# Performance work log

Measured on AMD Instinct MI355X. Metric: run time of the kernel, lower is better.

## Reference

```python
import jax, jax.numpy as jnp
import numpy as np

N_NODES = 100000
N_EDGES = 1600000
IN_DIM = 128
HID = 128


def sage_conv(x, src, dst, W_l, W_r, b, num_nodes):
    # PyG SAGEConv (mean aggregation): out = lin_l(mean_{j in N(i)} x_j) + lin_r(x_i)
    msgs = x[src]                                            # [E, F] gather
    agg = jax.ops.segment_sum(msgs, dst, num_segments=num_nodes)  # [N, F]
    cnt = jax.ops.segment_sum(jnp.ones((src.shape[0],), x.dtype), dst,
                              num_segments=num_nodes)        # [N]
    agg = agg / jnp.maximum(cnt, 1.0)[:, None]               # mean; 0 for isolated nodes
    return agg @ W_l + b + x @ W_r


def setup_inputs() -> dict:
    key = jax.random.key(0)
    ks = jax.random.split(key, 12)
    s_in = 1.0 / np.sqrt(IN_DIM)
    s_h = 1.0 / np.sqrt(HID)
    return {
        "x": jax.random.normal(ks[0], (N_NODES, IN_DIM), jnp.float32),
        "edge_index": jax.random.randint(ks[1], (2, N_EDGES), 0, N_NODES, jnp.int64),
        "Wl1": jax.random.normal(ks[2], (IN_DIM, HID), jnp.float32) * s_in,
        "Wr1": jax.random.normal(ks[3], (IN_DIM, HID), jnp.float32) * s_in,
        "b1": jnp.zeros((HID,), jnp.float32),
        "Wl2": jax.random.normal(ks[4], (HID, HID), jnp.float32) * s_h,
        "Wr2": jax.random.normal(ks[5], (HID, HID), jnp.float32) * s_h,
        "b2": jnp.zeros((HID,), jnp.float32),
        "Wp": jax.random.normal(ks[6], (HID, 1), jnp.float32) * s_h,
        "bp": jnp.zeros((1,), jnp.float32),
        "Wd": jax.random.normal(ks[7], (HID, 1), jnp.float32) * s_h,
        "bd": jnp.zeros((1,), jnp.float32),
    }


def reference(x, edge_index, Wl1, Wr1, b1, Wl2, Wr2, b2, Wp, bp, Wd, bd):
    src, dst = edge_index[0], edge_index[1]
    h = jax.nn.relu(sage_conv(x, src, dst, Wl1, Wr1, b1, N_NODES))
    h = jax.nn.relu(sage_conv(h, src, dst, Wl2, Wr2, b2, N_NODES))
    preds = h @ Wp + bp                      # [N, 1]
    diffs = jax.nn.sigmoid(h @ Wd + bd)      # [N, 1]
    return (preds - diffs, preds + diffs)
```

## Files before the change

kernel.cpp:

```cpp
#include <hip/hip_runtime.h>
#include <hip/hip_bf16.h>

#define N_NODES 100000
#define N_EDGES 1600000
#define NBUCK 391
#define BCAP 5120
#define ACHUNK 4096

typedef __bf16 bf16x8 __attribute__((ext_vector_type(8)));
typedef __bf16 bf16x4 __attribute__((ext_vector_type(4)));
typedef float  f32x4  __attribute__((ext_vector_type(4)));
typedef float  f32x2  __attribute__((ext_vector_type(2)));



__global__ __launch_bounds__(512) void zerob_kernel(int* __restrict__ bcnt,
                                                    int* __restrict__ Psent) {
  int t = threadIdx.x;
  if (t < NBUCK) bcnt[t] = 0;
  if (t >= 480) Psent[t - 480] = 0;
}

__global__ __launch_bounds__(256) void partA_kernel(const int* __restrict__ src,
                                                    const int* __restrict__ dst,
                                                    int* __restrict__ bcnt,
                                                    unsigned* __restrict__ packed, int E) {
  __shared__ int hist[NBUCK];
  __shared__ int curs[NBUCK];
  const int t = threadIdx.x;
  for (int i = t; i < NBUCK; i += 256) hist[i] = 0;
  __syncthreads();

  const int base = blockIdx.x * ACHUNK;
  const int lim = min(base + ACHUNK, E);

  int dloc[16], sloc[16];
  int myn = 0;
  for (int i = base + t; i < lim; i += 256) {
    dloc[myn] = dst[i];
    sloc[myn] = src[i];
    ++myn;
  }
  for (int k = 0; k < myn; ++k) atomicAdd(&hist[dloc[k] >> 8], 1);
  __syncthreads();

  for (int i = t; i < NBUCK; i += 256) {
    int h = hist[i];
    curs[i] = (h > 0) ? atomicAdd(&bcnt[i], h) : 0;
  }
  __syncthreads();

  for (int k = 0; k < myn; ++k) {
    int d = dloc[k];
    int b = d >> 8;
    int pos = atomicAdd(&curs[b], 1);
    if (pos < BCAP)
      packed[(size_t)b * BCAP + pos] = ((unsigned)sloc[k] << 8) | (unsigned)(d & 255);
  }
}

__global__ __launch_bounds__(256) void partBh_kernel(const unsigned* __restrict__ packed,
                                                     const int* __restrict__ bcnt,
                                                     int* __restrict__ pcnt,
                                                     int* __restrict__ deg,
                                                     int* __restrict__ pbt, int N) {
  __shared__ int hist[256];
  __shared__ int red[256];
  const int b = blockIdx.x, t = threadIdx.x;
  hist[t] = 0;
  __syncthreads();
  const int ecnt = min(bcnt[b], BCAP);
  const unsigned* pk = packed + (size_t)b * BCAP;
  for (int i = t; i < ecnt; i += 256) atomicAdd(&hist[pk[i] & 255u], 1);
  __syncthreads();
  int c = hist[t];
  int node = b * 256 + t;
  int pc = (node < N) ? ((c + 3) & ~3) : 0;
  if (node < N) { deg[node] = c; pcnt[node] = pc; }
  red[t] = pc;
  __syncthreads();
  for (int d = 128; d > 0; d >>= 1) {
    if (t < d) red[t] += red[t + d];
    __syncthreads();
  }
  if (t == 0) pbt[b] = red[0];
}

__global__ __launch_bounds__(512) void bscan_kernel(const int* __restrict__ pbt,
                                                    int* __restrict__ bbase,
                                                    int* __restrict__ offs, int N) {
  __shared__ int tmp[512];
  int t = threadIdx.x;
  int v = (t < NBUCK) ? pbt[t] : 0;
  int x = v;
  tmp[t] = x;
  __syncthreads();
  for (int d = 1; d < 512; d <<= 1) {
    int y = (t >= d) ? tmp[t - d] : 0;
    __syncthreads();
    x += y;
    tmp[t] = x;
    __syncthreads();
  }
  if (t < NBUCK) bbase[t] = x - v;
  if (t == NBUCK - 1) offs[N] = x;
}

__global__ __launch_bounds__(256) void partBs_kernel(const unsigned* __restrict__ packed,
                                                     const int* __restrict__ bcnt,
                                                     const int* __restrict__ bbase,
                                                     const int* __restrict__ pcnt,
                                                     const int* __restrict__ deg,
                                                     int* __restrict__ offs,
                                                     int* __restrict__ ssrc, int N) {
  __shared__ int scanbuf[256];
  __shared__ int curs[256];
  const int b = blockIdx.x, t = threadIdx.x;
  const int node = b * 256 + t;
  int pc = (node < N) ? pcnt[node] : 0;
  int c  = (node < N) ? deg[node] : 0;
  int x = pc;
  scanbuf[t] = x;
  __syncthreads();
  for (int d = 1; d < 256; d <<= 1) {
    int y = (t >= d) ? scanbuf[t - d] : 0;
    __syncthreads();
    x += y;
    scanbuf[t] = x;
    __syncthreads();
  }
  int excl = x - pc;
  const int obase = bbase[b];
  if (node < N) offs[node] = obase + excl;
  curs[t] = excl;
  __syncthreads();

  const int ecnt = min(bcnt[b], BCAP);
  const unsigned* pk = packed + (size_t)b * BCAP;
  for (int i = t; i < ecnt; i += 256) {
    unsigned p = pk[i];
    int r = atomicAdd(&curs[p & 255u], 1);
    ssrc[obase + r] = (int)(p >> 8);
  }
  for (int j = c; j < pc; ++j) ssrc[obase + excl + j] = N;
}


__global__ __launch_bounds__(256) void wswz_kernel(const float* __restrict__ Wl1,
                                                   const float* __restrict__ Wr1,
                                                   const float* __restrict__ Wl2,
                                                   const float* __restrict__ Wr2,
                                                   __bf16* __restrict__ W1out,
                                                   __bf16* __restrict__ W2out) {
  int gi = blockIdx.x * blockDim.x + threadIdx.x;
  bool L2 = gi >= 32768;
  int i = gi & 32767;
  int j = i & 7;
  int lane = (i >> 3) & 63;
  int c = (i >> 9) & 3;
  int tile = i >> 11;
  int k = c * 32 + ((lane >> 4) * 8) + j;
  int krow = L2 ? (((k & 7) << 4) | (k >> 3)) : k;
  int col = tile * 16 + (lane & 15);
  const float* Wl = L2 ? Wl2 : Wl1;
  const float* Wr = L2 ? Wr2 : Wr1;
  float v = (col < 128) ? Wl[krow * 128 + col] : Wr[krow * 128 + (col - 128)];
  (L2 ? W2out : W1out)[i] = (__bf16)v;
}


template <bool A_IS_F32>
__global__ __launch_bounds__(256) void gemm_kernel(const void* __restrict__ Aptr,
                                                   const __bf16* __restrict__ Wswz,
                                                   const float* __restrict__ bias,
                                                   unsigned char* __restrict__ P,
                                                   __bf16* __restrict__ R, int M) {
  __shared__ __bf16 ldsA[64][136];
  const int t = threadIdx.x;
  const int m0 = blockIdx.x * 64;

  if (A_IS_F32) {
    const float* A = (const float*)Aptr;
#pragma unroll
    for (int it = 0; it < 8; ++it) {
      int row = it * 8 + (t >> 5);
      int col = (t & 31) * 4;
      float4 v = make_float4(0.f, 0.f, 0.f, 0.f);
      if (m0 + row < M) v = *(const float4*)&A[(size_t)(m0 + row) * 128 + col];
      bf16x4 bv;
      bv.x = (__bf16)v.x; bv.y = (__bf16)v.y; bv.z = (__bf16)v.z; bv.w = (__bf16)v.w;
      *(bf16x4*)&ldsA[row][col] = bv;
    }
  } else {
    const __bf16* A = (const __bf16*)Aptr;
#pragma unroll
    for (int it = 0; it < 4; ++it) {
      int row = it * 16 + (t >> 4);
      int col = (t & 15) * 8;
      uint4 v = make_uint4(0u, 0u, 0u, 0u);
      if (m0 + row < M) v = *(const uint4*)&A[(size_t)(m0 + row) * 128 + col];
      *(uint4*)&ldsA[row][col] = v;
    }
  }

  const int lane = t & 63;
  const int w = t >> 6;
  const int q = lane >> 4;
  const int s = lane & 15;

  float breg[8];
#pragma unroll
  for (int j = 0; j < 8; ++j) breg[j] = bias[j * 16 + s];

  __syncthreads();

  f32x4 acc[16];
  f32x4 zero = {0.f, 0.f, 0.f, 0.f};
#pragma unroll
  for (int i = 0; i < 16; ++i) acc[i] = zero;

  const __bf16* arow = &ldsA[w * 16 + s][0];
#pragma unroll
  for (int c = 0; c < 4; ++c) {
    bf16x8 a = *(const bf16x8*)&arow[c * 32 + q * 8];
#pragma unroll
    for (int nt = 0; nt < 16; ++nt) {
      bf16x8 b = *(const bf16x8*)&Wswz[(size_t)(((nt * 4 + c) * 64) + lane) * 8];
      acc[nt] = __builtin_amdgcn_mfma_f32_16x16x32_bf16(a, b, acc[nt], 0, 0, 0);
    }
  }

  const int rbase = m0 + w * 16 + q * 4;
#pragma unroll
  for (int r = 0; r < 4; ++r) {
    int row = rbase + r;
    if (row < M) {
      unsigned lo = 0, hi = 0;
      lo = __builtin_amdgcn_cvt_pk_fp8_f32(acc[0][r], acc[1][r], lo, false);
      lo = __builtin_amdgcn_cvt_pk_fp8_f32(acc[2][r], acc[3][r], lo, true);
      hi = __builtin_amdgcn_cvt_pk_fp8_f32(acc[4][r], acc[5][r], hi, false);
      hi = __builtin_amdgcn_cvt_pk_fp8_f32(acc[6][r], acc[7][r], hi, true);
      uint2 pv; pv.x = lo; pv.y = hi;
      *(uint2*)&P[(size_t)row * 128 + s * 8] = pv;

      bf16x8 o;
#pragma unroll
      for (int j = 0; j < 8; ++j) o[j] = (__bf16)(acc[8 + j][r] + breg[j]);
      *(bf16x8*)&R[(size_t)row * 128 + s * 8] = o;
    }
  }
}


template <bool FINAL>
__global__ __launch_bounds__(256) void agg_kernel(
    const unsigned char* __restrict__ P, const __bf16* R,
    const int* __restrict__ offs, const int* __restrict__ deg,
    const int* __restrict__ ssrc,
    __bf16* H, float* __restrict__ out,
    const float* __restrict__ Wp, const float* __restrict__ Wd,
    const float* __restrict__ bp, const float* __restrict__ bd, int n) {
  int w4 = (int)((blockIdx.x * blockDim.x + threadIdx.x) >> 6);
  int lane = threadIdx.x & 63;
  int g = lane >> 4;
  int s = lane & 15;
  int node = w4 * 4 + g;
  int nc = min(node, n - 1);
  int start = offs[nc];
  int pend = offs[nc + 1];

  f32x2 a01 = {0.f, 0.f}, a23 = {0.f, 0.f}, a45 = {0.f, 0.f}, a67 = {0.f, 0.f};

  const unsigned char* Pb = P + (size_t)s * 8;
  for (int cur = start; cur < pend; cur += 4) {
    uint4 sv = *(const uint4*)&ssrc[cur];
    uint2 v0 = *(const uint2*)(Pb + (size_t)sv.x * 128);
    uint2 v1 = *(const uint2*)(Pb + (size_t)sv.y * 128);
    uint2 v2 = *(const uint2*)(Pb + (size_t)sv.z * 128);
    uint2 v3 = *(const uint2*)(Pb + (size_t)sv.w * 128);
    a01 += __builtin_amdgcn_cvt_pk_f32_fp8(v0.x, false);
    a23 += __builtin_amdgcn_cvt_pk_f32_fp8(v0.x, true);
    a45 += __builtin_amdgcn_cvt_pk_f32_fp8(v0.y, false);
    a67 += __builtin_amdgcn_cvt_pk_f32_fp8(v0.y, true);
    a01 += __builtin_amdgcn_cvt_pk_f32_fp8(v1.x, false);
    a23 += __builtin_amdgcn_cvt_pk_f32_fp8(v1.x, true);
    a45 += __builtin_amdgcn_cvt_pk_f32_fp8(v1.y, false);
    a67 += __builtin_amdgcn_cvt_pk_f32_fp8(v1.y, true);
    a01 += __builtin_amdgcn_cvt_pk_f32_fp8(v2.x, false);
    a23 += __builtin_amdgcn_cvt_pk_f32_fp8(v2.x, true);
    a45 += __builtin_amdgcn_cvt_pk_f32_fp8(v2.y, false);
    a67 += __builtin_amdgcn_cvt_pk_f32_fp8(v2.y, true);
    a01 += __builtin_amdgcn_cvt_pk_f32_fp8(v3.x, false);
    a23 += __builtin_amdgcn_cvt_pk_f32_fp8(v3.x, true);
    a45 += __builtin_amdgcn_cvt_pk_f32_fp8(v3.y, false);
    a67 += __builtin_amdgcn_cvt_pk_f32_fp8(v3.y, true);
  }

  int dg = deg[nc];
  float inv = 1.0f / (float)(dg > 0 ? dg : 1);

  bf16x8 rv = *(const bf16x8*)&R[(size_t)nc * 128 + s * 8];
  float acc[8] = {a01[0], a01[1], a23[0], a23[1], a45[0], a45[1], a67[0], a67[1]};
  float h[8];
#pragma unroll
  for (int j = 0; j < 8; ++j) {
    h[j] = fmaxf(acc[j] * inv + (float)rv[j], 0.f);
  }

  if (!FINAL) {
    if (node < n) {
      bf16x8 o;
#pragma unroll
      for (int j = 0; j < 8; ++j) o[j] = (__bf16)h[j];
      *(bf16x8*)&H[(size_t)node * 128 + s * 8] = o;
    }
  } else {
    float p = 0.f, dd = 0.f;
#pragma unroll
    for (int j = 0; j < 8; ++j) {
      p += h[j] * Wp[j * 16 + s];
      dd += h[j] * Wd[j * 16 + s];
    }
    p += __shfl_xor(p, 1, 64);  p += __shfl_xor(p, 2, 64);
    p += __shfl_xor(p, 4, 64);  p += __shfl_xor(p, 8, 64);
    dd += __shfl_xor(dd, 1, 64); dd += __shfl_xor(dd, 2, 64);
    dd += __shfl_xor(dd, 4, 64); dd += __shfl_xor(dd, 8, 64);
    if (node < n && s == 0) {
      float preds = p + bp[0];
      float sg = 1.0f / (1.0f + __expf(-(dd + bd[0])));
      out[node] = preds - sg;
      out[n + node] = preds + sg;
    }
  }
}


extern "C" void kernel_launch(void* const* d_in, const int* in_sizes, int n_in,
                              void* d_out, int out_size, void* d_ws, size_t ws_size,
                              hipStream_t stream) {
  const float* x    = (const float*)d_in[0];
  const int*   ei   = (const int*)d_in[1];
  const float* Wl1 = (const float*)d_in[2];
  const float* Wr1 = (const float*)d_in[3];
  const float* b1  = (const float*)d_in[4];
  const float* Wl2 = (const float*)d_in[5];
  const float* Wr2 = (const float*)d_in[6];
  const float* b2  = (const float*)d_in[7];
  const float* Wp  = (const float*)d_in[8];
  const float* bp  = (const float*)d_in[9];
  const float* Wd  = (const float*)d_in[10];
  const float* bd  = (const float*)d_in[11];
  float* out = (float*)d_out;

  const int N = N_NODES, E = N_EDGES;
  const int* src = ei;
  const int* dst = ei + E;
  const size_t PADE = (size_t)E + 3 * (size_t)N + 64;

  char* w = (char*)d_ws;
  unsigned char* P = (unsigned char*)w; w += (size_t)(N + 1) * 128;
  __bf16* Rbuf   = (__bf16*)w;   w += (size_t)N * 128 * 2;
  int* ssrc      = (int*)w;      w += PADE * 4;
  unsigned* pck  = (unsigned*)w; w += (size_t)NBUCK * BCAP * 4;
  int* bcnt      = (int*)w;      w += 512 * 4;
  int* bbase     = (int*)w;      w += 512 * 4;
  int* pbt       = (int*)w;      w += 512 * 4;
  int* pcnt      = (int*)w;      w += (size_t)(N + 32) * 4;
  int* deg       = (int*)w;      w += (size_t)(N + 32) * 4;
  int* offs      = (int*)w;      w += (size_t)(N + 32) * 4;
  __bf16* Ws1    = (__bf16*)w;   w += 65536;
  __bf16* Ws2    = (__bf16*)w;   w += 65536;

  zerob_kernel<<<1, 512, 0, stream>>>(bcnt, (int*)(P + (size_t)N * 128));
  wswz_kernel<<<256, 256, 0, stream>>>(Wl1, Wr1, Wl2, Wr2, Ws1, Ws2);
  partA_kernel<<<(E + ACHUNK - 1) / ACHUNK, 256, 0, stream>>>(src, dst, bcnt, pck, E);
  partBh_kernel<<<NBUCK, 256, 0, stream>>>(pck, bcnt, pcnt, deg, pbt, N);
  bscan_kernel<<<1, 512, 0, stream>>>(pbt, bbase, offs, N);
  partBs_kernel<<<NBUCK, 256, 0, stream>>>(pck, bcnt, bbase, pcnt, deg, offs, ssrc, N);

  const int GB = (N + 63) / 64;
  const int AB = (N + 15) / 16;
  gemm_kernel<true><<<GB, 256, 0, stream>>>(x, Ws1, b1, P, Rbuf, N);
  agg_kernel<false><<<AB, 256, 0, stream>>>(P, Rbuf, offs, deg, ssrc, Rbuf, nullptr,
                                            nullptr, nullptr, nullptr, nullptr, N);
  gemm_kernel<false><<<GB, 256, 0, stream>>>(Rbuf, Ws2, b2, P, Rbuf, N);
  agg_kernel<true><<<AB, 256, 0, stream>>>(P, Rbuf, offs, deg, ssrc, nullptr, out,
                                           Wp, Wd, bp, bd, N);
}
```

Measured before the change: 275.8 us.

## Make GEMM persistent with register-resident weight fragments per wave

The GEMM now launches a fixed grid of 512 blocks that loop over 64-row tiles. Each wave loads its 64-column slice of the swizzled weights into registers once and reuses it for every tile, instead of re-reading weights from global memory for each tile. A-operand fragments are read directly from global memory into registers, bypassing LDS and the block barrier. Outputs are split so waves 0-1 write the fp8 P half and waves 2-3 write the bf16 R half. Because each block now reads A rows that other blocks may be writing, the second GEMM gets its own R2 buffer, costing extra workspace. Register pressure is higher, and occupancy is set with launch_bounds(256,2).

Result: no change. 278.9 us (+1.1%).

```diff
diff --git a/kernel.cpp b/kernel.cpp
--- a/kernel.cpp
+++ b/kernel.cpp
@@ -170,83 +170,95 @@
 
 
 template <bool A_IS_F32>
-__global__ __launch_bounds__(256) void gemm_kernel(const void* __restrict__ Aptr,
-                                                   const __bf16* __restrict__ Wswz,
-                                                   const float* __restrict__ bias,
-                                                   unsigned char* __restrict__ P,
-                                                   __bf16* __restrict__ R, int M) {
-  __shared__ __bf16 ldsA[64][136];
+__global__ __launch_bounds__(256, 2) void gemm_kernel(const void* __restrict__ Aptr,
+                                                      const __bf16* __restrict__ Wswz,
+                                                      const float* __restrict__ bias,
+                                                      unsigned char* __restrict__ P,
+                                                      __bf16* __restrict__ R, int M,
+                                                      int tiles, int stride) {
   const int t = threadIdx.x;
-  const int m0 = blockIdx.x * 64;
-
-  if (A_IS_F32) {
-    const float* A = (const float*)Aptr;
-#pragma unroll
-    for (int it = 0; it < 8; ++it) {
-      int row = it * 8 + (t >> 5);
-      int col = (t & 31) * 4;
-      float4 v = make_float4(0.f, 0.f, 0.f, 0.f);
-      if (m0 + row < M) v = *(const float4*)&A[(size_t)(m0 + row) * 128 + col];
-      bf16x4 bv;
-      bv.x = (__bf16)v.x; bv.y = (__bf16)v.y; bv.z = (__bf16)v.z; bv.w = (__bf16)v.w;
-      *(bf16x4*)&ldsA[row][col] = bv;
-    }
-  } else {
-    const __bf16* A = (const __bf16*)Aptr;
-#pragma unroll
-    for (int it = 0; it < 4; ++it) {
-      int row = it * 16 + (t >> 4);
-      int col = (t & 15) * 8;
-      uint4 v = make_uint4(0u, 0u, 0u, 0u);
-      if (m0 + row < M) v = *(const uint4*)&A[(size_t)(m0 + row) * 128 + col];
-      *(uint4*)&ldsA[row][col] = v;
-    }
-  }
-
   const int lane = t & 63;
   const int w = t >> 6;
   const int q = lane >> 4;
   const int s = lane & 15;
 
-  float breg[8];
-#pragma unroll
-  for (int j = 0; j < 8; ++j) breg[j] = bias[j * 16 + s];
-
-  __syncthreads();
-
-  f32x4 acc[16];
-  f32x4 zero = {0.f, 0.f, 0.f, 0.f};
-#pragma unroll
-  for (int i = 0; i < 16; ++i) acc[i] = zero;
-
-  const __bf16* arow = &ldsA[w * 16 + s][0];
-#pragma unroll
-  for (int c = 0; c < 4; ++c) {
-    bf16x8 a = *(const bf16x8*)&arow[c * 32 + q * 8];
-#pragma unroll
-    for (int nt = 0; nt < 16; ++nt) {
-      bf16x8 b = *(const bf16x8*)&Wswz[(size_t)(((nt * 4 + c) * 64) + lane) * 8];
-      acc[nt] = __builtin_amdgcn_mfma_f32_16x16x32_bf16(a, b, acc[nt], 0, 0, 0);
+  bf16x8 bfrag[16];
+#pragma unroll
+  for (int ct = 0; ct < 4; ++ct)
+#pragma unroll
+    for (int c = 0; c < 4; ++c)
+      bfrag[ct * 4 + c] =
+          *(const bf16x8*)&Wswz[(size_t)((((w * 4 + ct) * 4 + c) * 64) + lane) * 8];
+
+  float breg[4];
+#pragma unroll
+  for (int j = 0; j < 4; ++j)
+    breg[j] = (w >= 2) ? bias[((w - 2) * 4 + j) * 16 + s] : 0.f;
+
+  for (int tile = blockIdx.x; tile < tiles; tile += stride) {
+    const int m0 = tile * 64;
+
+    bf16x8 afrag[16];
+    if (A_IS_F32) {
+      const float* A = (const float*)Aptr;
+#pragma unroll
+      for (int rt = 0; rt < 4; ++rt) {
+        int rc = min(m0 + rt * 16 + s, M - 1);
+#pragma unroll
+        for (int c = 0; c < 4; ++c) {
+          const float* p = &A[(size_t)rc * 128 + c * 32 + q * 8];
+          float4 v0 = *(const float4*)p;
+          float4 v1 = *(const float4*)(p + 4);
+          bf16x8 a;
+          a[0] = (__bf16)v0.x; a[1] = (__bf16)v0.y; a[2] = (__bf16)v0.z; a[3] = (__bf16)v0.w;
+          a[4] = (__bf16)v1.x; a[5] = (__bf16)v1.y; a[6] = (__bf16)v1.z; a[7] = (__bf16)v1.w;
+          afrag[rt * 4 + c] = a;
+        }
+      }
+    } else {
+      const __bf16* A = (const __bf16*)Aptr;
+#pragma unroll
+      for (int rt = 0; rt < 4; ++rt) {
+        int rc = min(m0 + rt * 16 + s, M - 1);
+#pragma unroll
+        for (int c = 0; c < 4; ++c)
+          afrag[rt * 4 + c] = *(const bf16x8*)&A[(size_t)rc * 128 + c * 32 + q * 8];
+      }
     }
-  }
-
-  const int rbase = m0 + w * 16 + q * 4;
-#pragma unroll
-  for (int r = 0; r < 4; ++r) {
-    int row = rbase + r;
-    if (row < M) {
-      unsigned lo = 0, hi = 0;
-      lo = __builtin_amdgcn_cvt_pk_fp8_f32(acc[0][r], acc[1][r], lo, false);
-      lo = __builtin_amdgcn_cvt_pk_fp8_f32(acc[2][r], acc[3][r], lo, true);
-      hi = __builtin_amdgcn_cvt_pk_fp8_f32(acc[4][r], acc[5][r], hi, false);
-      hi = __builtin_amdgcn_cvt_pk_fp8_f32(acc[6][r], acc[7][r], hi, true);
-      uint2 pv; pv.x = lo; pv.y = hi;
-      *(uint2*)&P[(size_t)row * 128 + s * 8] = pv;
-
-      bf16x8 o;
-#pragma unroll
-      for (int j = 0; j < 8; ++j) o[j] = (__bf16)(acc[8 + j][r] + breg[j]);
-      *(bf16x8*)&R[(size_t)row * 128 + s * 8] = o;
+
+    f32x4 acc[16];
+    f32x4 zero = {0.f, 0.f, 0.f, 0.f};
+#pragma unroll
+    for (int i = 0; i < 16; ++i) acc[i] = zero;
+
+#pragma unroll
+    for (int c = 0; c < 4; ++c)
+#pragma unroll
+      for (int rt = 0; rt < 4; ++rt)
+#pragma unroll
+        for (int ct = 0; ct < 4; ++ct)
+          acc[rt * 4 + ct] = __builtin_amdgcn_mfma_f32_16x16x32_bf16(
+              afrag[rt * 4 + c], bfrag[ct * 4 + c], acc[rt * 4 + ct], 0, 0, 0);
+
+#pragma unroll
+    for (int rt = 0; rt < 4; ++rt) {
+#pragma unroll
+      for (int r = 0; r < 4; ++r) {
+        int row = m0 + rt * 16 + q * 4 + r;
+        if (row < M) {
+          if (w < 2) {
+            unsigned v = 0;
+            v = __builtin_amdgcn_cvt_pk_fp8_f32(acc[rt * 4 + 0][r], acc[rt * 4 + 1][r], v, false);
+            v = __builtin_amdgcn_cvt_pk_fp8_f32(acc[rt * 4 + 2][r], acc[rt * 4 + 3][r], v, true);
+            *(unsigned*)&P[(size_t)row * 128 + s * 8 + w * 4] = v;
+          } else {
+            bf16x4 o;
+#pragma unroll
+            for (int ct = 0; ct < 4; ++ct) o[ct] = (__bf16)(acc[rt * 4 + ct][r] + breg[ct]);
+            *(bf16x4*)&R[(size_t)row * 128 + s * 8 + (w - 2) * 4] = o;
+          }
+        }
+      }
     }
   }
 }
@@ -359,7 +371,8 @@
 
   char* w = (char*)d_ws;
   unsigned char* P = (unsigned char*)w; w += (size_t)(N + 1) * 128;
-  __bf16* Rbuf   = (__bf16*)w;   w += (size_t)N * 128 * 2;
+  __bf16* R1     = (__bf16*)w;   w += (size_t)N * 128 * 2;
+  __bf16* R2     = (__bf16*)w;   w += (size_t)N * 128 * 2;
   int* ssrc      = (int*)w;      w += PADE * 4;
   unsigned* pck  = (unsigned*)w; w += (size_t)NBUCK * BCAP * 4;
   int* bcnt      = (int*)w;      w += 512 * 4;
@@ -378,12 +391,13 @@
   bscan_kernel<<<1, 512, 0, stream>>>(pbt, bbase, offs, N);
   partBs_kernel<<<NBUCK, 256, 0, stream>>>(pck, bcnt, bbase, pcnt, deg, offs, ssrc, N);
 
-  const int GB = (N + 63) / 64;
+  const int TILES = (N + 63) / 64;
+  const int GG = 512;
   const int AB = (N + 15) / 16;
-  gemm_kernel<true><<<GB, 256, 0, stream>>>(x, Ws1, b1, P, Rbuf, N);
-  agg_kernel<false><<<AB, 256, 0, stream>>>(P, Rbuf, offs, deg, ssrc, Rbuf, nullptr,
+  gemm_kernel<true><<<GG, 256, 0, stream>>>(x, Ws1, b1, P, R1, N, TILES, GG);
+  agg_kernel<false><<<AB, 256, 0, stream>>>(P, R1, offs, deg, ssrc, R1, nullptr,
                                             nullptr, nullptr, nullptr, nullptr, N);
-  gemm_kernel<false><<<GB, 256, 0, stream>>>(Rbuf, Ws2, b2, P, Rbuf, N);
-  agg_kernel<true><<<AB, 256, 0, stream>>>(P, Rbuf, offs, deg, ssrc, nullptr, out,
+  gemm_kernel<false><<<GG, 256, 0, stream>>>(R1, Ws2, b2, P, R2, N, TILES, GG);
+  agg_kernel<true><<<AB, 256, 0, stream>>>(P, R2, offs, deg, ssrc, nullptr, out,
                                            Wp, Wd, bp, bd, N);
 }
```
